# Kernel tuning notes

Hardware: AMD Instinct MI355X
Metric: run time of the kernel (lower is better)

The kernel has to match this reference:

```python
import jax, jax.numpy as jnp
import numpy as np
from jax import lax

# Module constraint: hidden_dim == state_dim == expand_dim (see broadcasting in original).
H = 128  # hidden_dim
N = 128  # state_dim
E = 128  # expand_dim = hidden_dim * expand_factor (expand_factor=1)
B, L = 4, 1024


def setup_inputs() -> dict:
    key = jax.random.key(0)
    ks = jax.random.split(key, 11)
    s = lambda fan: 1.0 / np.sqrt(fan)
    return {
        "u": jax.random.normal(ks[0], (B, L, H), jnp.float32),
        "W_in": jax.random.normal(ks[1], (H, 2 * E), jnp.float32) * s(H),
        "b_in": jax.random.normal(ks[2], (2 * E,), jnp.float32) * 0.01,
        "conv_w": jax.random.normal(ks[3], (E, 1, 3), jnp.float32) * s(3),
        "conv_b": jax.random.normal(ks[4], (E,), jnp.float32) * 0.01,
        "W_x": jax.random.normal(ks[5], (E, N + N + H), jnp.float32) * s(E),
        "b_x": jax.random.normal(ks[6], (N + N + H,), jnp.float32) * 0.01,
        "A_log": jax.random.normal(ks[7], (N,), jnp.float32),
        "D": jnp.ones((H,), jnp.float32),
        "W_out": jax.random.normal(ks[8], (E, H), jnp.float32) * s(E),
        "b_out": jax.random.normal(ks[9], (H,), jnp.float32) * 0.01,
    }


def reference(u, W_in, b_in, conv_w, conv_b, W_x, b_x, A_log, D, W_out, b_out):
    b, l, _ = u.shape
    xz = u @ W_in + b_in                       # [B,L,2E]
    x, z = jnp.split(xz, 2, axis=-1)           # [B,L,E] each
    # depthwise conv1d, kernel 3, padding 1 (groups == channels)
    xc = lax.conv_general_dilated(
        x.transpose(0, 2, 1), conv_w, window_strides=(1,), padding=[(1, 1)],
        feature_group_count=E, dimension_numbers=("NCH", "OIH", "NCH"))
    x = jax.nn.silu(xc.transpose(0, 2, 1) + conv_b)  # [B,L,E]
    ssm = x @ W_x + b_x                        # [B,L,2N+H]
    delta = jax.nn.softplus(ssm[..., :N])      # [B,L,N]
    Bm = ssm[..., N:2 * N]                     # [B,L,N]
    C = ssm[..., 2 * N:]                       # [B,L,H]
    A = -jnp.exp(A_log)                        # [N]

    def step(h, inp):
        d_t, B_t, C_t, x_t, u_t = inp          # [B,N],[B,N],[B,H],[B,E],[B,H]
        # A_discrete[b,t,i,j] = exp(delta[b,t,i] * A[j])  (outer broadcast, as in source)
        A_disc = jnp.exp(d_t[:, :, None] * A[None, None, :])       # [B,N,N]
        h = A_disc * h + (d_t * B_t)[:, :, None] * x_t[:, None, :]  # [B,N,E]
        y = (h * C_t[:, None, :]).sum(axis=1) + D * u_t             # [B,H]
        return h, y

    h0 = jnp.zeros((b, N, H), u.dtype)
    inputs = (delta.transpose(1, 0, 2), Bm.transpose(1, 0, 2),
              C.transpose(1, 0, 2), x.transpose(1, 0, 2), u.transpose(1, 0, 2))
    _, ys = lax.scan(step, h0, inputs)         # ys: [L,B,H]
    y = ys.transpose(1, 0, 2) * jax.nn.silu(z)  # [B,L,H] (E==H)
    return y @ W_out + b_out                   # dropout in eval mode: identity
```

## Files before the change

kernel.cpp:

```cpp
#include <hip/hip_runtime.h>
#include <hip/hip_bf16.h>

using bf16 = __hip_bfloat16;
typedef __attribute__((ext_vector_type(8))) short short8;
typedef __attribute__((ext_vector_type(4))) float f32x4;

#define BVAL 4
#define LVAL 1024
#define LOG2E 1.44269504f

#define TSEG 64
#define SSEG 16
#define CH   16
#define RST  132

#define OFF_U      0
#define OFF_WIN    524288
#define OFF_BIN    557056
#define OFF_CONVW  557312
#define OFF_CONVB  557696
#define OFF_WX     557824
#define OFF_BX     606976
#define OFF_ALOG   607360
#define OFF_D      607488
#define OFF_WOUT   607616
#define OFF_BOUT   624000
#define CVT_TOTAL  624128
#define FP32N      (CVT_TOTAL - OFF_WIN)

#define CVT2_U   524288
#define CVT2_WI  (CVT2_U + 32768)
#define CVT2_WX  (CVT2_WI + 49152)
#define CVT2_TOT (CVT2_WX + 16384)

__device__ __forceinline__ int dtype_flag(const void* D) {
    return ((*(const unsigned int*)D) & 0xFFFFu) != 0u ? 1 : 0;
}
__device__ __forceinline__ float ldin(const void* p, size_t i, int f) {
    return f ? __bfloat162float(((const bf16*)p)[i]) : ((const float*)p)[i];
}

__global__ void kcvt_all(const void* __restrict__ u, const void* __restrict__ W_in,
                         const void* __restrict__ b_in, const void* __restrict__ conv_w,
                         const void* __restrict__ conv_b, const void* __restrict__ W_x,
                         const void* __restrict__ b_x, const void* __restrict__ A_log,
                         const void* __restrict__ D, const void* __restrict__ W_out,
                         const void* __restrict__ b_out, float* __restrict__ dst,
                         bf16* __restrict__ ubf, bf16* __restrict__ wtin,
                         bf16* __restrict__ wtx, bf16* __restrict__ wtout) {
    int gidx = blockIdx.x * 256 + threadIdx.x;
    int f = dtype_flag(D);
    if (gidx < FP32N) {
        int idx = gidx + OFF_WIN;
        const void* p; int loc;
        if      (idx < OFF_BIN)   { p = W_in;   loc = idx - OFF_WIN; }
        else if (idx < OFF_CONVW) { p = b_in;   loc = idx - OFF_BIN; }
        else if (idx < OFF_CONVB) { p = conv_w; loc = idx - OFF_CONVW; }
        else if (idx < OFF_WX)    { p = conv_b; loc = idx - OFF_CONVB; }
        else if (idx < OFF_BX)    { p = W_x;    loc = idx - OFF_WX; }
        else if (idx < OFF_ALOG)  { p = b_x;    loc = idx - OFF_BX; }
        else if (idx < OFF_D)     { p = A_log;  loc = idx - OFF_ALOG; }
        else if (idx < OFF_WOUT)  { p = D;      loc = idx - OFF_D; }
        else if (idx < OFF_BOUT)  { p = W_out;  loc = idx - OFF_WOUT; }
        else                      { p = b_out;  loc = idx - OFF_BOUT; }
        dst[idx] = ldin(p, loc, f);
    } else {
        int ix = gidx - FP32N;
        if (ix >= CVT2_TOT) return;
        if (ix < CVT2_U) {
            ubf[ix] = __float2bfloat16(ldin(u, ix, f));
        } else if (ix < CVT2_WI) {
            int rel = ix - CVT2_U; int n = rel >> 7, k = rel & 127;
            wtin[rel] = __float2bfloat16(ldin(W_in, k * 256 + n, f));
        } else if (ix < CVT2_WX) {
            int rel = ix - CVT2_WI; int n = rel >> 7, k = rel & 127;
            wtx[rel] = __float2bfloat16(ldin(W_x, k * 384 + n, f));
        } else {
            int rel = ix - CVT2_WX; int n = rel >> 7, k = rel & 127;
            wtout[rel] = __float2bfloat16(ldin(W_out, k * 128 + n, f));
        }
    }
}

__global__ void k1_mfma(const bf16* __restrict__ ubf, const bf16* __restrict__ wtin,
                        const float* __restrict__ cvt,
                        float* __restrict__ x_pre, bf16* __restrict__ zsbf) {
    int blk = blockIdx.x, mb = blk >> 3, cb = blk & 7;
    int tid = threadIdx.x, w = tid >> 6, lane = tid & 63;
    int quad = lane >> 4, sub = lane & 15;
    int m0 = mb * 64 + w * 16, c = cb * 16;
    f32x4 accX = {0.f, 0.f, 0.f, 0.f}, accZ = {0.f, 0.f, 0.f, 0.f};
    #pragma unroll
    for (int ks = 0; ks < 4; ++ks) {
        int k0 = ks * 32 + quad * 8;
        short8 a  = *(const short8*)(ubf + (size_t)(m0 + sub) * 128 + k0);
        short8 bX = *(const short8*)(wtin + (size_t)(c + sub) * 128 + k0);
        short8 bZ = *(const short8*)(wtin + (size_t)(128 + c + sub) * 128 + k0);
        accX = __builtin_amdgcn_mfma_f32_16x16x32_bf16(a, bX, accX, 0, 0, 0);
        accZ = __builtin_amdgcn_mfma_f32_16x16x32_bf16(a, bZ, accZ, 0, 0, 0);
    }
    int o = c + sub;
    float bx_ = cvt[OFF_BIN + o], bz_ = cvt[OFF_BIN + 128 + o];
    #pragma unroll
    for (int r = 0; r < 4; ++r) {
        int m = m0 + quad * 4 + r;
        float x = accX[r] + bx_;
        float z = accZ[r] + bz_;
        x_pre[(size_t)m * 128 + o] = x;
        zsbf[(size_t)m * 128 + o] = __float2bfloat16(z / (1.0f + __expf(-z)));
    }
}

__global__ void k2_conv(const float* __restrict__ cvt, const float* __restrict__ x_pre,
                        float* __restrict__ xs, bf16* __restrict__ xsbf) {
    const float* conv_w = cvt + OFF_CONVW;
    const float* conv_b = cvt + OFF_CONVB;
    int q = blockIdx.x * 256 + threadIdx.x;
    int basee = q * 4;
    int row = basee >> 7;
    int l = row & (LVAL - 1);
    int e = basee & 127;
    float4 xc = *(const float4*)(x_pre + basee);
    float4 xm = make_float4(0.f, 0.f, 0.f, 0.f);
    float4 xp = make_float4(0.f, 0.f, 0.f, 0.f);
    if (l > 0)        xm = *(const float4*)(x_pre + basee - 128);
    if (l < LVAL - 1) xp = *(const float4*)(x_pre + basee + 128);
    float mm[4] = {xm.x, xm.y, xm.z, xm.w};
    float cc[4] = {xc.x, xc.y, xc.z, xc.w};
    float pp[4] = {xp.x, xp.y, xp.z, xp.w};
    float out[4];
    #pragma unroll
    for (int i = 0; i < 4; ++i) {
        float w0 = conv_w[(e + i) * 3 + 0];
        float w1 = conv_w[(e + i) * 3 + 1];
        float w2 = conv_w[(e + i) * 3 + 2];
        float v = fmaf(w0, mm[i], fmaf(w1, cc[i], fmaf(w2, pp[i], conv_b[e + i])));
        out[i] = v / (1.0f + __expf(-v));
    }
    *(float4*)(xs + basee) = make_float4(out[0], out[1], out[2], out[3]);
    #pragma unroll
    for (int i = 0; i < 4; ++i) xsbf[basee + i] = __float2bfloat16(out[i]);
}

__global__ void k3_mfma(const bf16* __restrict__ xsbf, const bf16* __restrict__ wtx,
                        const float* __restrict__ cvt,
                        float* __restrict__ delta, float* __restrict__ dB,
                        float* __restrict__ Cc) {
    int blk = blockIdx.x, mb = blk >> 3, cb = blk & 7;
    int tid = threadIdx.x, w = tid >> 6, lane = tid & 63;
    int quad = lane >> 4, sub = lane & 15;
    int m0 = mb * 64 + w * 16, c = cb * 16;
    f32x4 accA = {0.f,0.f,0.f,0.f}, accB = {0.f,0.f,0.f,0.f}, accC = {0.f,0.f,0.f,0.f};
    #pragma unroll
    for (int ks = 0; ks < 4; ++ks) {
        int k0 = ks * 32 + quad * 8;
        short8 a  = *(const short8*)(xsbf + (size_t)(m0 + sub) * 128 + k0);
        short8 bA = *(const short8*)(wtx + (size_t)(c + sub) * 128 + k0);
        short8 bB = *(const short8*)(wtx + (size_t)(128 + c + sub) * 128 + k0);
        short8 bC = *(const short8*)(wtx + (size_t)(256 + c + sub) * 128 + k0);
        accA = __builtin_amdgcn_mfma_f32_16x16x32_bf16(a, bA, accA, 0, 0, 0);
        accB = __builtin_amdgcn_mfma_f32_16x16x32_bf16(a, bB, accB, 0, 0, 0);
        accC = __builtin_amdgcn_mfma_f32_16x16x32_bf16(a, bC, accC, 0, 0, 0);
    }
    int o = c + sub;
    float ba = cvt[OFF_BX + o], bb = cvt[OFF_BX + 128 + o], bc = cvt[OFF_BX + 256 + o];
    #pragma unroll
    for (int r = 0; r < 4; ++r) {
        int m = m0 + quad * 4 + r;
        size_t idx = (size_t)m * 128 + o;
        float d = accA[r] + ba;
        float sp = (d > 20.0f) ? d : log1pf(__expf(d));
        delta[idx] = sp;
        dB[idx] = sp * (accB[r] + bb);
        Cc[idx] = accC[r] + bc;
    }
}


__global__ __launch_bounds__(256, 4)
void k5a(const float* __restrict__ cvt, const float* __restrict__ delta,
         const float* __restrict__ dB, const float* __restrict__ xs,
         float* __restrict__ hout, float* __restrict__ Pout) {
    __shared__ float sdl[CH * RST], swl[CH * RST];
    __shared__ float sx[TSEG][8];
    int blk = blockIdx.x;
    int b = blk >> 8, s = (blk >> 4) & 15, jg = blk & 15;
    int tid = threadIdx.x, w = tid >> 6, lane = tid & 63;
    int cj = lane >> 5, ln = lane & 31;
    int jj = w * 2 + cj, j = jg * 8 + jj;
    int t0 = s * TSEG;
    size_t base = (size_t)b * (LVAL * 128);
    {
        #pragma unroll
        for (int i = 0; i < 2; ++i) {
            int q = i * 256 + tid;
            int t = q >> 3, jc = q & 7;
            sx[t][jc] = xs[base + (size_t)(t0 + t) * 128 + jg * 8 + jc];
        }
    }
    float a2 = -__expf(cvt[OFF_ALOG + j]) * LOG2E;
    const float4* gd4 = (const float4*)(delta + base);
    const float4* gw4 = (const float4*)(dB + base);
    int fb = t0 * 32;
    float4 rd[2], rw[2];
    rd[0] = gd4[fb + tid]; rd[1] = gd4[fb + 256 + tid];
    rw[0] = gw4[fb + tid]; rw[1] = gw4[fb + 256 + tid];
    float h[4] = {0.f, 0.f, 0.f, 0.f};
    float p[4] = {1.f, 1.f, 1.f, 1.f};
    for (int c4 = 0; c4 < 4; ++c4) {
        #pragma unroll
        for (int i = 0; i < 2; ++i) {
            int q = i * 256 + tid;
            int t = q >> 5, c4i = q & 31;
            *(float4*)&sdl[t * RST + 4 * c4i] = rd[i];
            *(float4*)&swl[t * RST + 4 * c4i] = rw[i];
        }
        __syncthreads();
        if (c4 < 3) {
            int f2 = fb + (c4 + 1) * 512;
            rd[0] = gd4[f2 + tid]; rd[1] = gd4[f2 + 256 + tid];
            rw[0] = gw4[f2 + tid]; rw[1] = gw4[f2 + 256 + tid];
        }
        #pragma unroll 4
        for (int k = 0; k < CH; ++k) {
            int bl = k * RST + 4 * ln;
            float4 d = *(const float4*)&sdl[bl];
            float4 wv = *(const float4*)&swl[bl];
            float xv = sx[c4 * CH + k][jj];
            float e;
            e = exp2f(d.x * a2); h[0] = fmaf(e, h[0], wv.x * xv); p[0] *= e;
            e = exp2f(d.y * a2); h[1] = fmaf(e, h[1], wv.y * xv); p[1] *= e;
            e = exp2f(d.z * a2); h[2] = fmaf(e, h[2], wv.z * xv); p[2] *= e;
            e = exp2f(d.w * a2); h[3] = fmaf(e, h[3], wv.w * xv); p[3] *= e;
        }
        __syncthreads();
    }
    size_t cb = (((size_t)(b * SSEG + s) * 128 + j) * 128) + 4 * ln;
    *(float4*)(hout + cb) = make_float4(h[0], h[1], h[2], h[3]);
    *(float4*)(Pout + cb) = make_float4(p[0], p[1], p[2], p[3]);
}

__global__ __launch_bounds__(256, 4)
void k5c(const float* __restrict__ cvt, const float* __restrict__ delta,
         const float* __restrict__ dB, const float* __restrict__ Cc,
         const float* __restrict__ xs, const bf16* __restrict__ zsbf,
         const void* __restrict__ uin, const void* __restrict__ Din,
         const float* __restrict__ hout, const float* __restrict__ Pout,
         bf16* __restrict__ y2bf) {
    __shared__ float sdl[CH * RST], swl[CH * RST];
    __shared__ float sx[TSEG][8], sc[TSEG][8], su[TSEG][8], sz[TSEG][8];
    __shared__ float sy[TSEG][8];
    int blk = blockIdx.x;
    int b = blk >> 8, s = (blk >> 4) & 15, jg = blk & 15;
    int tid = threadIdx.x, w = tid >> 6, lane = tid & 63;
    int cj = lane >> 5, ln = lane & 31;
    int jj = w * 2 + cj, j = jg * 8 + jj;
    int t0 = s * TSEG;
    int f = dtype_flag(Din);
    size_t base = (size_t)b * (LVAL * 128);
    {
        #pragma unroll
        for (int i = 0; i < 2; ++i) {
            int q = i * 256 + tid;
            int t = q >> 3, jc = q & 7;
            size_t g = base + (size_t)(t0 + t) * 128 + jg * 8 + jc;
            sx[t][jc] = xs[g];
            sc[t][jc] = Cc[g];
            su[t][jc] = ldin(uin, g, f);
            sz[t][jc] = __bfloat162float(zsbf[g]);
        }
    }
    float a2 = -__expf(cvt[OFF_ALOG + j]) * LOG2E;
    float Dj = cvt[OFF_D + j];
    const float4* gd4 = (const float4*)(delta + base);
    const float4* gw4 = (const float4*)(dB + base);
    int fb = t0 * 32;
    float4 rd[2], rw[2];
    rd[0] = gd4[fb + tid]; rd[1] = gd4[fb + 256 + tid];
    rw[0] = gw4[fb + tid]; rw[1] = gw4[fb + 256 + tid];
    float h[4] = {0.f, 0.f, 0.f, 0.f};
    size_t cstep = (size_t)128 * 128;
    size_t cb0 = (((size_t)(b * SSEG) * 128 + j) * 128) + 4 * ln;
    for (int sp = 0; sp < s; ++sp) {
        size_t cb = cb0 + (size_t)sp * cstep;
        float4 ho = *(const float4*)(hout + cb);
        float4 pp = *(const float4*)(Pout + cb);
        h[0] = fmaf(pp.x, h[0], ho.x); h[1] = fmaf(pp.y, h[1], ho.y);
        h[2] = fmaf(pp.z, h[2], ho.z); h[3] = fmaf(pp.w, h[3], ho.w);
    }
    for (int c4 = 0; c4 < 4; ++c4) {
        #pragma unroll
        for (int i = 0; i < 2; ++i) {
            int q = i * 256 + tid;
            int t = q >> 5, c4i = q & 31;
            *(float4*)&sdl[t * RST + 4 * c4i] = rd[i];
            *(float4*)&swl[t * RST + 4 * c4i] = rw[i];
        }
        __syncthreads();
        if (c4 < 3) {
            int f2 = fb + (c4 + 1) * 512;
            rd[0] = gd4[f2 + tid]; rd[1] = gd4[f2 + 256 + tid];
            rw[0] = gw4[f2 + tid]; rw[1] = gw4[f2 + 256 + tid];
        }
        #pragma unroll 4
        for (int k = 0; k < CH; ++k) {
            int bl = k * RST + 4 * ln;
            float4 d = *(const float4*)&sdl[bl];
            float4 wv = *(const float4*)&swl[bl];
            int t = c4 * CH + k;
            float xv = sx[t][jj];
            float e;
            e = exp2f(d.x * a2); h[0] = fmaf(e, h[0], wv.x * xv);
            e = exp2f(d.y * a2); h[1] = fmaf(e, h[1], wv.y * xv);
            e = exp2f(d.z * a2); h[2] = fmaf(e, h[2], wv.z * xv);
            e = exp2f(d.w * a2); h[3] = fmaf(e, h[3], wv.w * xv);
            float sm = (h[0] + h[1]) + (h[2] + h[3]);
            sm += __shfl_xor(sm, 1, 64);
            sm += __shfl_xor(sm, 2, 64);
            sm += __shfl_xor(sm, 4, 64);
            sm += __shfl_xor(sm, 8, 64);
            sm += __shfl_xor(sm, 16, 64);
            if (ln == 0) {
                float y = fmaf(sc[t][jj], sm, Dj * su[t][jj]);
                sy[t][jj] = y * sz[t][jj];
            }
        }
        __syncthreads();
    }
    #pragma unroll
    for (int i = 0; i < 2; ++i) {
        int q = i * 256 + tid;
        int t = q >> 3, jc = q & 7;
        y2bf[base + (size_t)(t0 + t) * 128 + jg * 8 + jc] = __float2bfloat16(sy[t][jc]);
    }
}

__global__ void k6_mfma(const bf16* __restrict__ y2bf, const bf16* __restrict__ wtout,
                        const float* __restrict__ cvt, const void* __restrict__ Din,
                        void* __restrict__ out) {
    int blk = blockIdx.x, mb = blk >> 2, nb = blk & 3;
    int tid = threadIdx.x, w = tid >> 6, lane = tid & 63;
    int quad = lane >> 4, sub = lane & 15;
    int m0 = mb * 64 + w * 16, n0 = nb * 32;
    f32x4 acc0 = {0.f,0.f,0.f,0.f}, acc1 = {0.f,0.f,0.f,0.f};
    #pragma unroll
    for (int ks = 0; ks < 4; ++ks) {
        int k0 = ks * 32 + quad * 8;
        short8 a  = *(const short8*)(y2bf + (size_t)(m0 + sub) * 128 + k0);
        short8 b0 = *(const short8*)(wtout + (size_t)(n0 + sub) * 128 + k0);
        short8 b1 = *(const short8*)(wtout + (size_t)(n0 + 16 + sub) * 128 + k0);
        acc0 = __builtin_amdgcn_mfma_f32_16x16x32_bf16(a, b0, acc0, 0, 0, 0);
        acc1 = __builtin_amdgcn_mfma_f32_16x16x32_bf16(a, b1, acc1, 0, 0, 0);
    }
    int f = dtype_flag(Din);
    float bo0 = cvt[OFF_BOUT + n0 + sub], bo1 = cvt[OFF_BOUT + n0 + 16 + sub];
    #pragma unroll
    for (int r = 0; r < 4; ++r) {
        int m = m0 + quad * 4 + r;
        float v0 = acc0[r] + bo0, v1 = acc1[r] + bo1;
        if (f) {
            ((bf16*)out)[(size_t)m * 128 + n0 + sub] = __float2bfloat16(v0);
            ((bf16*)out)[(size_t)m * 128 + n0 + 16 + sub] = __float2bfloat16(v1);
        } else {
            ((float*)out)[(size_t)m * 128 + n0 + sub] = v0;
            ((float*)out)[(size_t)m * 128 + n0 + 16 + sub] = v1;
        }
    }
}

extern "C" void kernel_launch(void* const* d_in, const int* in_sizes, int n_in,
                              void* d_out, int out_size, void* d_ws, size_t ws_size,
                              hipStream_t stream) {
    const size_t NE = (size_t)BVAL * LVAL * 128;
    const size_t NC = (size_t)BVAL * SSEG * 128 * 128;

    float* cvt   = (float*)d_ws;
    float* bufs  = cvt + CVT_TOTAL;
    float* x_pre = bufs + 0 * NE;
    float* zsb   = bufs + 1 * NE;
    float* xs    = bufs + 2 * NE;
    float* delta = bufs + 3 * NE;
    float* dB    = bufs + 4 * NE;
    float* Cc    = bufs + 5 * NE;
    float* hout  = bufs + 6 * NE;
    float* Pou   = hout + NC;
    float* bfarea = Pou + NC;
    bf16* zsbf  = (bf16*)zsb;
    bf16* ubf   = (bf16*)bfarea;
    bf16* xsbf  = ubf + NE;
    bf16* y2bf  = xsbf + NE;
    bf16* wtin  = y2bf + NE;
    bf16* wtx   = wtin + 32768;
    bf16* wtout = wtx + 49152;

    const int ROWS = BVAL * LVAL;
    const int CVT_ALL = FP32N + CVT2_TOT;

    kcvt_all<<<(CVT_ALL + 255) / 256, 256, 0, stream>>>(
        d_in[0], d_in[1], d_in[2], d_in[3], d_in[4], d_in[5],
        d_in[6], d_in[7], d_in[8], d_in[9], d_in[10],
        cvt, ubf, wtin, wtx, wtout);
    k1_mfma<<<512, 256, 0, stream>>>(ubf, wtin, cvt, x_pre, zsbf);
    k2_conv<<<(ROWS * 128) / (256 * 4), 256, 0, stream>>>(cvt, x_pre, xs, xsbf);
    k3_mfma<<<512, 256, 0, stream>>>(xsbf, wtx, cvt, delta, dB, Cc);
    k5a<<<BVAL * SSEG * 16, 256, 0, stream>>>(cvt, delta, dB, xs, hout, Pou);
    k5c<<<BVAL * SSEG * 16, 256, 0, stream>>>(cvt, delta, dB, Cc, xs, zsbf,
                                              d_in[0], d_in[8], hout, Pou, y2bf);
    k6_mfma<<<256, 256, 0, stream>>>(y2bf, wtout, cvt, d_in[8], d_out);
}
```

Measured before the change: 171.5 us.

## Read scan inputs directly from global and batch per-step reductions through LDS

The scan kernels stop staging delta and dB through padded shared-memory tiles and instead load float4 values straight from global memory per step, which removes those block-wide barriers and LDS traffic. In k5a the running decay product is replaced by a sum of deltas that is exponentiated once at the end. In k5c the per-step five-level shuffle reduction is replaced by writing partial sums to a per-wave LDS tile and reducing 16 steps at once with vector loads plus a single shuffle. The cost is more uncached-looking global loads inside the serial loop, and the exp-of-sum form differs numerically from the product.

```diff
diff --git a/kernel.cpp b/kernel.cpp
--- a/kernel.cpp
+++ b/kernel.cpp
@@ -12,7 +12,7 @@
 #define TSEG 64
 #define SSEG 16
 #define CH   16
-#define RST  132
+#define YST  72
 
 #define OFF_U      0
 #define OFF_WIN    524288
@@ -181,7 +181,6 @@
 void k5a(const float* __restrict__ cvt, const float* __restrict__ delta,
          const float* __restrict__ dB, const float* __restrict__ xs,
          float* __restrict__ hout, float* __restrict__ Pout) {
-    __shared__ float sdl[CH * RST], swl[CH * RST];
     __shared__ float sx[TSEG][8];
     int blk = blockIdx.x;
     int b = blk >> 8, s = (blk >> 4) & 15, jg = blk & 15;
@@ -190,54 +189,37 @@
     int jj = w * 2 + cj, j = jg * 8 + jj;
     int t0 = s * TSEG;
     size_t base = (size_t)b * (LVAL * 128);
-    {
-        #pragma unroll
-        for (int i = 0; i < 2; ++i) {
-            int q = i * 256 + tid;
-            int t = q >> 3, jc = q & 7;
-            sx[t][jc] = xs[base + (size_t)(t0 + t) * 128 + jg * 8 + jc];
-        }
-    }
+    #pragma unroll
+    for (int i = 0; i < 2; ++i) {
+        int q = i * 256 + tid;
+        int t = q >> 3, jc = q & 7;
+        sx[t][jc] = xs[base + (size_t)(t0 + t) * 128 + jg * 8 + jc];
+    }
+    __syncthreads();
     float a2 = -__expf(cvt[OFF_ALOG + j]) * LOG2E;
-    const float4* gd4 = (const float4*)(delta + base);
-    const float4* gw4 = (const float4*)(dB + base);
-    int fb = t0 * 32;
-    float4 rd[2], rw[2];
-    rd[0] = gd4[fb + tid]; rd[1] = gd4[fb + 256 + tid];
-    rw[0] = gw4[fb + tid]; rw[1] = gw4[fb + 256 + tid];
+    const float4* dp = (const float4*)(delta + base) + (size_t)t0 * 32 + ln;
+    const float4* wp = (const float4*)(dB + base) + (size_t)t0 * 32 + ln;
     float h[4] = {0.f, 0.f, 0.f, 0.f};
-    float p[4] = {1.f, 1.f, 1.f, 1.f};
+    float sd[4] = {0.f, 0.f, 0.f, 0.f};
     for (int c4 = 0; c4 < 4; ++c4) {
-        #pragma unroll
-        for (int i = 0; i < 2; ++i) {
-            int q = i * 256 + tid;
-            int t = q >> 5, c4i = q & 31;
-            *(float4*)&sdl[t * RST + 4 * c4i] = rd[i];
-            *(float4*)&swl[t * RST + 4 * c4i] = rw[i];
-        }
-        __syncthreads();
-        if (c4 < 3) {
-            int f2 = fb + (c4 + 1) * 512;
-            rd[0] = gd4[f2 + tid]; rd[1] = gd4[f2 + 256 + tid];
-            rw[0] = gw4[f2 + tid]; rw[1] = gw4[f2 + 256 + tid];
-        }
         #pragma unroll 4
         for (int k = 0; k < CH; ++k) {
-            int bl = k * RST + 4 * ln;
-            float4 d = *(const float4*)&sdl[bl];
-            float4 wv = *(const float4*)&swl[bl];
-            float xv = sx[c4 * CH + k][jj];
+            int t = c4 * CH + k;
+            float4 d  = dp[(size_t)t * 32];
+            float4 wv = wp[(size_t)t * 32];
+            float xv = sx[t][jj];
             float e;
-            e = exp2f(d.x * a2); h[0] = fmaf(e, h[0], wv.x * xv); p[0] *= e;
-            e = exp2f(d.y * a2); h[1] = fmaf(e, h[1], wv.y * xv); p[1] *= e;
-            e = exp2f(d.z * a2); h[2] = fmaf(e, h[2], wv.z * xv); p[2] *= e;
-            e = exp2f(d.w * a2); h[3] = fmaf(e, h[3], wv.w * xv); p[3] *= e;
+            e = exp2f(d.x * a2); h[0] = fmaf(e, h[0], wv.x * xv); sd[0] += d.x;
+            e = exp2f(d.y * a2); h[1] = fmaf(e, h[1], wv.y * xv); sd[1] += d.y;
+            e = exp2f(d.z * a2); h[2] = fmaf(e, h[2], wv.z * xv); sd[2] += d.z;
+            e = exp2f(d.w * a2); h[3] = fmaf(e, h[3], wv.w * xv); sd[3] += d.w;
         }
         __syncthreads();
     }
     size_t cb = (((size_t)(b * SSEG + s) * 128 + j) * 128) + 4 * ln;
     *(float4*)(hout + cb) = make_float4(h[0], h[1], h[2], h[3]);
-    *(float4*)(Pout + cb) = make_float4(p[0], p[1], p[2], p[3]);
+    *(float4*)(Pout + cb) = make_float4(exp2f(sd[0] * a2), exp2f(sd[1] * a2),
+                                        exp2f(sd[2] * a2), exp2f(sd[3] * a2));
 }
 
 __global__ __launch_bounds__(256, 4)
@@ -247,9 +229,9 @@
          const void* __restrict__ uin, const void* __restrict__ Din,
          const float* __restrict__ hout, const float* __restrict__ Pout,
          bf16* __restrict__ y2bf) {
-    __shared__ float sdl[CH * RST], swl[CH * RST];
     __shared__ float sx[TSEG][8], sc[TSEG][8], su[TSEG][8], sz[TSEG][8];
-    __shared__ float sy[TSEG][8];
+    __shared__ float yt[4][CH * YST];
+    __shared__ float sy[TSEG][9];
     int blk = blockIdx.x;
     int b = blk >> 8, s = (blk >> 4) & 15, jg = blk & 15;
     int tid = threadIdx.x, w = tid >> 6, lane = tid & 63;
@@ -258,26 +240,19 @@
     int t0 = s * TSEG;
     int f = dtype_flag(Din);
     size_t base = (size_t)b * (LVAL * 128);
-    {
-        #pragma unroll
-        for (int i = 0; i < 2; ++i) {
-            int q = i * 256 + tid;
-            int t = q >> 3, jc = q & 7;
-            size_t g = base + (size_t)(t0 + t) * 128 + jg * 8 + jc;
-            sx[t][jc] = xs[g];
-            sc[t][jc] = Cc[g];
-            su[t][jc] = ldin(uin, g, f);
-            sz[t][jc] = __bfloat162float(zsbf[g]);
-        }
-    }
+    #pragma unroll
+    for (int i = 0; i < 2; ++i) {
+        int q = i * 256 + tid;
+        int t = q >> 3, jc = q & 7;
+        size_t g = base + (size_t)(t0 + t) * 128 + jg * 8 + jc;
+        sx[t][jc] = xs[g];
+        sc[t][jc] = Cc[g];
+        su[t][jc] = ldin(uin, g, f);
+        sz[t][jc] = __bfloat162float(zsbf[g]);
+    }
+    __syncthreads();
     float a2 = -__expf(cvt[OFF_ALOG + j]) * LOG2E;
     float Dj = cvt[OFF_D + j];
-    const float4* gd4 = (const float4*)(delta + base);
-    const float4* gw4 = (const float4*)(dB + base);
-    int fb = t0 * 32;
-    float4 rd[2], rw[2];
-    rd[0] = gd4[fb + tid]; rd[1] = gd4[fb + 256 + tid];
-    rw[0] = gw4[fb + tid]; rw[1] = gw4[fb + 256 + tid];
     float h[4] = {0.f, 0.f, 0.f, 0.f};
     size_t cstep = (size_t)128 * 128;
     size_t cb0 = (((size_t)(b * SSEG) * 128 + j) * 128) + 4 * ln;
@@ -288,41 +263,39 @@
         h[0] = fmaf(pp.x, h[0], ho.x); h[1] = fmaf(pp.y, h[1], ho.y);
         h[2] = fmaf(pp.z, h[2], ho.z); h[3] = fmaf(pp.w, h[3], ho.w);
     }
+    const float4* dp = (const float4*)(delta + base) + (size_t)t0 * 32 + ln;
+    const float4* wp = (const float4*)(dB + base) + (size_t)t0 * 32 + ln;
+    float* ytw = yt[w];
+    int rk = lane & 15, rc2 = lane >> 5, rhl = (lane >> 4) & 1;
     for (int c4 = 0; c4 < 4; ++c4) {
-        #pragma unroll
-        for (int i = 0; i < 2; ++i) {
-            int q = i * 256 + tid;
-            int t = q >> 5, c4i = q & 31;
-            *(float4*)&sdl[t * RST + 4 * c4i] = rd[i];
-            *(float4*)&swl[t * RST + 4 * c4i] = rw[i];
-        }
-        __syncthreads();
-        if (c4 < 3) {
-            int f2 = fb + (c4 + 1) * 512;
-            rd[0] = gd4[f2 + tid]; rd[1] = gd4[f2 + 256 + tid];
-            rw[0] = gw4[f2 + tid]; rw[1] = gw4[f2 + 256 + tid];
-        }
         #pragma unroll 4
         for (int k = 0; k < CH; ++k) {
-            int bl = k * RST + 4 * ln;
-            float4 d = *(const float4*)&sdl[bl];
-            float4 wv = *(const float4*)&swl[bl];
             int t = c4 * CH + k;
+            float4 d  = dp[(size_t)t * 32];
+            float4 wv = wp[(size_t)t * 32];
             float xv = sx[t][jj];
             float e;
             e = exp2f(d.x * a2); h[0] = fmaf(e, h[0], wv.x * xv);
             e = exp2f(d.y * a2); h[1] = fmaf(e, h[1], wv.y * xv);
             e = exp2f(d.z * a2); h[2] = fmaf(e, h[2], wv.z * xv);
             e = exp2f(d.w * a2); h[3] = fmaf(e, h[3], wv.w * xv);
-            float sm = (h[0] + h[1]) + (h[2] + h[3]);
-            sm += __shfl_xor(sm, 1, 64);
-            sm += __shfl_xor(sm, 2, 64);
-            sm += __shfl_xor(sm, 4, 64);
-            sm += __shfl_xor(sm, 8, 64);
+            ytw[k * YST + cj * 36 + ln] = (h[0] + h[1]) + (h[2] + h[3]);
+        }
+        __builtin_amdgcn_wave_barrier();
+        {
+            const float* rowp = &ytw[rk * YST + rc2 * 36 + rhl * 16];
+            float4 v0 = *(const float4*)(rowp + 0);
+            float4 v1 = *(const float4*)(rowp + 4);
+            float4 v2 = *(const float4*)(rowp + 8);
+            float4 v3 = *(const float4*)(rowp + 12);
+            float sm = (((v0.x + v0.y) + (v0.z + v0.w)) + ((v1.x + v1.y) + (v1.z + v1.w)))
+                     + (((v2.x + v2.y) + (v2.z + v2.w)) + ((v3.x + v3.y) + (v3.z + v3.w)));
             sm += __shfl_xor(sm, 16, 64);
-            if (ln == 0) {
-                float y = fmaf(sc[t][jj], sm, Dj * su[t][jj]);
-                sy[t][jj] = y * sz[t][jj];
+            if (rhl == 0) {
+                int t = c4 * CH + rk;
+                int jj2 = w * 2 + rc2;
+                float y = fmaf(sc[t][jj2], sm, Dj * su[t][jj2]);
+                sy[t][jj2] = y * sz[t][jj2];
             }
         }
         __syncthreads();
```

Measured after the change: 170.9 us. No clear change (-0.3%).
